# Performance work log

Hardware: AMD Instinct MI355X
Metric: run time of the kernel (lower is better)

Reference implementation:

```python
import jax, jax.numpy as jnp
import numpy as np

DT = 0.001  # forward's default dt
EPS = 1e-10


def setup_inputs() -> dict:
    key = jax.random.key(0)
    k1, k2 = jax.random.split(key)
    nt, ntr, nc = 4096, 1024, 3
    x = jax.random.normal(k1, (nt, ntr, nc), dtype=jnp.float32)
    y = jax.random.normal(k2, (nt, ntr, nc), dtype=jnp.float32)
    return {"x": x, "y": y}


def reference(x, y):
    # x, y: [nt, ntraces, nchannels]
    nt = x.shape[0]
    # autocorrelation energy per (trace, channel) column via Parseval-style FFT sum
    X = jnp.fft.fft(x, axis=0)
    Y = jnp.fft.fft(y, axis=0)
    Ex = DT * jnp.sum(jnp.abs(X) ** 2, axis=0) / nt + EPS  # [ntr, nc]
    Ey = DT * jnp.sum(jnp.abs(Y) ** 2, axis=0) / nt + EPS  # [ntr, nc]
    dots = jnp.sum(x * y, axis=0)                          # [ntr, nc]
    cc = dots / jnp.sqrt(Ex * Ey)                          # [ntr, nc]
    # original skips columns whose max |x| is exactly 0
    mask = jnp.max(jnp.abs(x), axis=0) > 0
    loss = jnp.sum(jnp.where(mask, cc, 0.0))
    return loss
```

## Files before the change

kernel.cpp:

```cpp
#include <hip/hip_runtime.h>


#define NT 4096
#define NCOL 3072
#define NCOL4 (NCOL / 4)
#define TCHUNKS 128
#define TSTEPS (NT / TCHUNKS)

__device__ __constant__ float c_dt = 0.001f;
__device__ __constant__ float c_eps = 1e-10f;

#define WS_FLOATS (4 * NCOL)

__global__ __launch_bounds__(256) void ncc_partial(const float* __restrict__ x,
                                                   const float* __restrict__ y,
                                                   float* __restrict__ ws) {
    const int g    = blockIdx.x % 3;
    const int tch  = blockIdx.x / 3;
    const int tid  = threadIdx.x;
    const int col4 = g * 256 + tid;
    const int j    = col4 * 4;

    const float4* __restrict__ x4 = reinterpret_cast<const float4*>(x);
    const float4* __restrict__ y4 = reinterpret_cast<const float4*>(y);

    float sx2[4] = {0.f, 0.f, 0.f, 0.f};
    float sy2[4] = {0.f, 0.f, 0.f, 0.f};
    float sxy[4] = {0.f, 0.f, 0.f, 0.f};
    float amx[4] = {0.f, 0.f, 0.f, 0.f};

    const int t0 = tch * TSTEPS;
#pragma unroll 4
    for (int tt = 0; tt < TSTEPS; ++tt) {
        const int idx = (t0 + tt) * NCOL4 + col4;
        float4 xv = x4[idx];
        float4 yv = y4[idx];
        sx2[0] = fmaf(xv.x, xv.x, sx2[0]);
        sx2[1] = fmaf(xv.y, xv.y, sx2[1]);
        sx2[2] = fmaf(xv.z, xv.z, sx2[2]);
        sx2[3] = fmaf(xv.w, xv.w, sx2[3]);
        sy2[0] = fmaf(yv.x, yv.x, sy2[0]);
        sy2[1] = fmaf(yv.y, yv.y, sy2[1]);
        sy2[2] = fmaf(yv.z, yv.z, sy2[2]);
        sy2[3] = fmaf(yv.w, yv.w, sy2[3]);
        sxy[0] = fmaf(xv.x, yv.x, sxy[0]);
        sxy[1] = fmaf(xv.y, yv.y, sxy[1]);
        sxy[2] = fmaf(xv.z, yv.z, sxy[2]);
        sxy[3] = fmaf(xv.w, yv.w, sxy[3]);
        amx[0] = fmaxf(amx[0], fabsf(xv.x));
        amx[1] = fmaxf(amx[1], fabsf(xv.y));
        amx[2] = fmaxf(amx[2], fabsf(xv.z));
        amx[3] = fmaxf(amx[3], fabsf(xv.w));
    }

    float* __restrict__ sx2w = ws;
    float* __restrict__ sy2w = ws + NCOL;
    float* __restrict__ sxyw = ws + 2 * NCOL;
    unsigned int* __restrict__ amxw = reinterpret_cast<unsigned int*>(ws + 3 * NCOL);

#pragma unroll
    for (int k = 0; k < 4; ++k) {
        atomicAdd(&sx2w[j + k], sx2[k]);
        atomicAdd(&sy2w[j + k], sy2[k]);
        atomicAdd(&sxyw[j + k], sxy[k]);
        atomicMax(&amxw[j + k], __float_as_uint(amx[k]));
    }
}

__global__ __launch_bounds__(1024) void ncc_final(const float* __restrict__ ws,
                                                  float* __restrict__ out) {
    const int tid = threadIdx.x;
    const float* __restrict__ sx2w = ws;
    const float* __restrict__ sy2w = ws + NCOL;
    const float* __restrict__ sxyw = ws + 2 * NCOL;
    const unsigned int* __restrict__ amxw =
        reinterpret_cast<const unsigned int*>(ws + 3 * NCOL);

    float acc = 0.f;
#pragma unroll
    for (int j = tid; j < NCOL; j += 1024) {
        float ex = fmaf(c_dt, sx2w[j], c_eps);
        float ey = fmaf(c_dt, sy2w[j], c_eps);
        float cc = sxyw[j] * rsqrtf(ex * ey);
        if (amxw[j] != 0u) acc += cc;
    }

#pragma unroll
    for (int off = 32; off > 0; off >>= 1)
        acc += __shfl_down(acc, off, 64);

    __shared__ float red[16];
    const int wave = tid >> 6;
    const int lane = tid & 63;
    if (lane == 0) red[wave] = acc;
    __syncthreads();
    if (wave == 0) {
        float v = (lane < 16) ? red[lane] : 0.f;
#pragma unroll
        for (int off = 8; off > 0; off >>= 1)
            v += __shfl_down(v, off, 64);
        if (lane == 0) out[0] = v;
    }
}

extern "C" void kernel_launch(void* const* d_in, const int* in_sizes, int n_in,
                              void* d_out, int out_size, void* d_ws, size_t ws_size,
                              hipStream_t stream) {
    const float* x = reinterpret_cast<const float*>(d_in[0]);
    const float* y = reinterpret_cast<const float*>(d_in[1]);
    float* out = reinterpret_cast<float*>(d_out);
    float* ws = reinterpret_cast<float*>(d_ws);

    hipMemsetAsync(ws, 0, WS_FLOATS * sizeof(float), stream);

    ncc_partial<<<dim3(3 * TCHUNKS), dim3(256), 0, stream>>>(x, y, ws);
    ncc_final<<<dim3(1), dim3(1024), 0, stream>>>(ws, out);
}
```

Baseline: 131.7 us.

## Replace atomic partial reduction with deterministic three-stage reduction, drop max-abs mask

Stage one now writes per-chunk partial sums to a workspace buffer instead of issuing global atomics, doubling the chunk count to 256. A second kernel sums the chunks per column and computes per-block correlation sums, and a third kernel adds those up. This removes the memset and atomic contention. It adds about 9 MB of partial-sum traffic and an extra launch. The max-abs mask is replaced by a test on sum of squares being positive, which is mathematically equivalent.

```diff
diff --git a/kernel.cpp b/kernel.cpp
--- a/kernel.cpp
+++ b/kernel.cpp
@@ -3,104 +3,100 @@
 
 #define NT 4096
 #define NCOL 3072
-#define NCOL4 (NCOL / 4)
-#define TCHUNKS 128
-#define TSTEPS (NT / TCHUNKS)
+#define NCOL4 768
+#define CHUNKS 256
+#define TSTEPS (NT / CHUNKS)
 
-__device__ __constant__ float c_dt = 0.001f;
-__device__ __constant__ float c_eps = 1e-10f;
+#define PS_F4_PER_STAT (CHUNKS * NCOL4)
+#define BSUM_OFFSET_BYTES (3 * PS_F4_PER_STAT * 16)
 
-#define WS_FLOATS (4 * NCOL)
-
-__global__ __launch_bounds__(256) void ncc_partial(const float* __restrict__ x,
-                                                   const float* __restrict__ y,
-                                                   float* __restrict__ ws) {
-    const int g    = blockIdx.x % 3;
-    const int tch  = blockIdx.x / 3;
+__global__ __launch_bounds__(256) void ncc_stage1(const float* __restrict__ x,
+                                                  const float* __restrict__ y,
+                                                  float4* __restrict__ ps) {
+    const int bx   = blockIdx.x;
+    const int g    = bx % 3;
+    const int ch   = bx / 3;
     const int tid  = threadIdx.x;
     const int col4 = g * 256 + tid;
-    const int j    = col4 * 4;
 
     const float4* __restrict__ x4 = reinterpret_cast<const float4*>(x);
     const float4* __restrict__ y4 = reinterpret_cast<const float4*>(y);
 
-    float sx2[4] = {0.f, 0.f, 0.f, 0.f};
-    float sy2[4] = {0.f, 0.f, 0.f, 0.f};
-    float sxy[4] = {0.f, 0.f, 0.f, 0.f};
-    float amx[4] = {0.f, 0.f, 0.f, 0.f};
+    float4 sx2 = {0.f, 0.f, 0.f, 0.f};
+    float4 sy2 = {0.f, 0.f, 0.f, 0.f};
+    float4 sxy = {0.f, 0.f, 0.f, 0.f};
 
-    const int t0 = tch * TSTEPS;
-#pragma unroll 4
+    const int t0 = ch * TSTEPS;
+#pragma unroll
     for (int tt = 0; tt < TSTEPS; ++tt) {
         const int idx = (t0 + tt) * NCOL4 + col4;
         float4 xv = x4[idx];
         float4 yv = y4[idx];
-        sx2[0] = fmaf(xv.x, xv.x, sx2[0]);
-        sx2[1] = fmaf(xv.y, xv.y, sx2[1]);
-        sx2[2] = fmaf(xv.z, xv.z, sx2[2]);
-        sx2[3] = fmaf(xv.w, xv.w, sx2[3]);
-        sy2[0] = fmaf(yv.x, yv.x, sy2[0]);
-        sy2[1] = fmaf(yv.y, yv.y, sy2[1]);
-        sy2[2] = fmaf(yv.z, yv.z, sy2[2]);
-        sy2[3] = fmaf(yv.w, yv.w, sy2[3]);
-        sxy[0] = fmaf(xv.x, yv.x, sxy[0]);
-        sxy[1] = fmaf(xv.y, yv.y, sxy[1]);
-        sxy[2] = fmaf(xv.z, yv.z, sxy[2]);
-        sxy[3] = fmaf(xv.w, yv.w, sxy[3]);
-        amx[0] = fmaxf(amx[0], fabsf(xv.x));
-        amx[1] = fmaxf(amx[1], fabsf(xv.y));
-        amx[2] = fmaxf(amx[2], fabsf(xv.z));
-        amx[3] = fmaxf(amx[3], fabsf(xv.w));
+        sx2.x = fmaf(xv.x, xv.x, sx2.x);
+        sx2.y = fmaf(xv.y, xv.y, sx2.y);
+        sx2.z = fmaf(xv.z, xv.z, sx2.z);
+        sx2.w = fmaf(xv.w, xv.w, sx2.w);
+        sy2.x = fmaf(yv.x, yv.x, sy2.x);
+        sy2.y = fmaf(yv.y, yv.y, sy2.y);
+        sy2.z = fmaf(yv.z, yv.z, sy2.z);
+        sy2.w = fmaf(yv.w, yv.w, sy2.w);
+        sxy.x = fmaf(xv.x, yv.x, sxy.x);
+        sxy.y = fmaf(xv.y, yv.y, sxy.y);
+        sxy.z = fmaf(xv.z, yv.z, sxy.z);
+        sxy.w = fmaf(xv.w, yv.w, sxy.w);
     }
 
-    float* __restrict__ sx2w = ws;
-    float* __restrict__ sy2w = ws + NCOL;
-    float* __restrict__ sxyw = ws + 2 * NCOL;
-    unsigned int* __restrict__ amxw = reinterpret_cast<unsigned int*>(ws + 3 * NCOL);
+    const int slot = ch * NCOL4 + col4;
+    ps[0 * PS_F4_PER_STAT + slot] = sx2;
+    ps[1 * PS_F4_PER_STAT + slot] = sy2;
+    ps[2 * PS_F4_PER_STAT + slot] = sxy;
+}
 
+__global__ __launch_bounds__(256) void ncc_stage2(const float* __restrict__ ps,
+                                                  float* __restrict__ bsum) {
+    const int b    = blockIdx.x;
+    const int tid  = threadIdx.x;
+    const int lane = tid & 63;
+    const int q    = tid >> 6;
+    const int j    = b * 64 + lane;
+
+    float sx2 = 0.f, sy2 = 0.f, sxy = 0.f;
+    const int c0 = q * (CHUNKS / 4);
+#pragma unroll 4
+    for (int c = c0; c < c0 + CHUNKS / 4; ++c) {
+        sx2 += ps[0 * CHUNKS * NCOL + c * NCOL + j];
+        sy2 += ps[1 * CHUNKS * NCOL + c * NCOL + j];
+        sxy += ps[2 * CHUNKS * NCOL + c * NCOL + j];
+    }
+
+    __shared__ float red[3][4][64];
+    red[0][q][lane] = sx2;
+    red[1][q][lane] = sy2;
+    red[2][q][lane] = sxy;
+    __syncthreads();
+
+    if (q == 0) {
+        sx2 = red[0][0][lane] + red[0][1][lane] + red[0][2][lane] + red[0][3][lane];
+        sy2 = red[1][0][lane] + red[1][1][lane] + red[1][2][lane] + red[1][3][lane];
+        sxy = red[2][0][lane] + red[2][1][lane] + red[2][2][lane] + red[2][3][lane];
+        float ex = fmaf(0.001f, sx2, 1e-10f);
+        float ey = fmaf(0.001f, sy2, 1e-10f);
+        float cc = (sx2 > 0.f) ? sxy * rsqrtf(ex * ey) : 0.f;
 #pragma unroll
-    for (int k = 0; k < 4; ++k) {
-        atomicAdd(&sx2w[j + k], sx2[k]);
-        atomicAdd(&sy2w[j + k], sy2[k]);
-        atomicAdd(&sxyw[j + k], sxy[k]);
-        atomicMax(&amxw[j + k], __float_as_uint(amx[k]));
+        for (int off = 32; off > 0; off >>= 1)
+            cc += __shfl_down(cc, off, 64);
+        if (lane == 0) bsum[b] = cc;
     }
 }
 
-__global__ __launch_bounds__(1024) void ncc_final(const float* __restrict__ ws,
-                                                  float* __restrict__ out) {
-    const int tid = threadIdx.x;
-    const float* __restrict__ sx2w = ws;
-    const float* __restrict__ sy2w = ws + NCOL;
-    const float* __restrict__ sxyw = ws + 2 * NCOL;
-    const unsigned int* __restrict__ amxw =
-        reinterpret_cast<const unsigned int*>(ws + 3 * NCOL);
-
-    float acc = 0.f;
-#pragma unroll
-    for (int j = tid; j < NCOL; j += 1024) {
-        float ex = fmaf(c_dt, sx2w[j], c_eps);
-        float ey = fmaf(c_dt, sy2w[j], c_eps);
-        float cc = sxyw[j] * rsqrtf(ex * ey);
-        if (amxw[j] != 0u) acc += cc;
-    }
-
+__global__ __launch_bounds__(64) void ncc_stage3(const float* __restrict__ bsum,
+                                                 float* __restrict__ out) {
+    const int lane = threadIdx.x;
+    float v = (lane < 48) ? bsum[lane] : 0.f;
 #pragma unroll
     for (int off = 32; off > 0; off >>= 1)
-        acc += __shfl_down(acc, off, 64);
-
-    __shared__ float red[16];
-    const int wave = tid >> 6;
-    const int lane = tid & 63;
-    if (lane == 0) red[wave] = acc;
-    __syncthreads();
-    if (wave == 0) {
-        float v = (lane < 16) ? red[lane] : 0.f;
-#pragma unroll
-        for (int off = 8; off > 0; off >>= 1)
-            v += __shfl_down(v, off, 64);
-        if (lane == 0) out[0] = v;
-    }
+        v += __shfl_down(v, off, 64);
+    if (lane == 0) out[0] = v;
 }
 
 extern "C" void kernel_launch(void* const* d_in, const int* in_sizes, int n_in,
@@ -109,10 +105,10 @@
     const float* x = reinterpret_cast<const float*>(d_in[0]);
     const float* y = reinterpret_cast<const float*>(d_in[1]);
     float* out = reinterpret_cast<float*>(d_out);
-    float* ws = reinterpret_cast<float*>(d_ws);
+    float4* ps = reinterpret_cast<float4*>(d_ws);
+    float* bsum = reinterpret_cast<float*>(reinterpret_cast<char*>(d_ws) + BSUM_OFFSET_BYTES);
 
-    hipMemsetAsync(ws, 0, WS_FLOATS * sizeof(float), stream);
-
-    ncc_partial<<<dim3(3 * TCHUNKS), dim3(256), 0, stream>>>(x, y, ws);
-    ncc_final<<<dim3(1), dim3(1024), 0, stream>>>(ws, out);
+    ncc_stage1<<<dim3(3 * CHUNKS), dim3(256), 0, stream>>>(x, y, ps);
+    ncc_stage2<<<dim3(48), dim3(256), 0, stream>>>(reinterpret_cast<const float*>(ps), bsum);
+    ncc_stage3<<<dim3(1), dim3(64), 0, stream>>>(bsum, out);
 }
```

Result: faster. 126.6 us (-3.9%).
